# Optimization experiments

Measured on AMD Instinct MI355X. Metric: run time of the kernel, lower is better.

## Reference

```python
import jax, jax.numpy as jnp
import numpy as np

THEA = 0.5
DELTA = 1.5
IGNORE = 255
K = 19  # num classes (len(weights))
LOSS_WEIGHT = 1.0
MIN_PIXELS = 20.0  # class kept only if pixel count > 20
WEIGHTS = jnp.ones((K,), dtype=jnp.float32)
EPS = 1e-12


def setup_inputs() -> dict:
    key = jax.random.key(0)
    k1, k2 = jax.random.split(key)
    n, c, h, w = 4, 32, 512, 1024
    predict = jax.random.normal(k1, (n, c, h, w), dtype=jnp.float32)
    target = jax.random.randint(k2, (n, h, w), 0, K, dtype=jnp.int32)
    return {"predict": predict, "target": target}


def _loss(predict, target):
    n, c, h, w = predict.shape
    # (n,c,h,w) -> (n*h*w, c), matching predict.permute(0,2,3,1)
    feat = jnp.transpose(predict, (0, 2, 3, 1)).reshape(-1, c)
    seg = target.reshape(-1)
    valid_pix = seg != IGNORE
    seg = jnp.where(valid_pix, seg, K).astype(jnp.int32)  # ignored -> extra segment K
    ones = valid_pix.astype(feat.dtype)

    # per-class counts and means (segment reduce replaces the python class loop)
    counts = jax.ops.segment_sum(ones, seg, num_segments=K + 1)[:K]
    sums = jax.ops.segment_sum(feat * ones[:, None], seg, num_segments=K + 1)[:K]
    centers = sums / jnp.maximum(counts, 1.0)[:, None]  # [K, c]
    valid_cls = counts > MIN_PIXELS
    n_cls = jnp.maximum(jnp.sum(valid_cls.astype(feat.dtype)), 1.0)

    # ---- variance term: relu(||mean - x|| - thea)^2, normalized by #positives ----
    ctr_ext = jnp.concatenate([centers, jnp.zeros((1, c), centers.dtype)], axis=0)
    ctr_pix = ctr_ext[seg]  # gather per-pixel center
    res = jnp.sqrt(jnp.sum((ctr_pix - feat) ** 2, axis=1) + EPS)  # [n*h*w]
    r = jax.nn.relu(res - THEA) * ones
    sq = jax.ops.segment_sum(r * r, seg, num_segments=K + 1)[:K]
    pos = jax.ops.segment_sum((r > 0).astype(feat.dtype), seg, num_segments=K + 1)[:K]
    norml = jnp.maximum(jax.lax.stop_gradient(pos), 1.0)  # numpy count in original: no grad
    loss_var = jnp.sum(jnp.where(valid_cls, WEIGHTS * sq / norml, 0.0)) / n_cls

    # ---- pairwise center distance term ----
    diff = centers[:, None, :] - centers[None, :, :]  # [K, K, c]
    dist = jnp.sqrt(jnp.sum(diff * diff, axis=-1) + EPS)
    pair_mask = valid_cls[:, None] & valid_cls[None, :] & ~jnp.eye(K, dtype=bool)
    d = jax.nn.relu(2.0 * DELTA - dist)
    loss_dis = jnp.sum(jnp.where(pair_mask, d * d, 0.0)) / jnp.maximum(n_cls * (n_cls - 1.0), 1.0)

    # ---- regularization term ----
    loss_reg = jnp.sum(jnp.where(valid_cls, jnp.sqrt(jnp.sum(centers * centers, axis=1) + EPS), 0.0)) / n_cls

    return LOSS_WEIGHT * (loss_var + loss_dis + 0.001 * loss_reg)


def reference(predict, target):
    return _loss(predict, target)
```

## Files before the change

kernel.cpp:

```cpp
#include <hip/hip_runtime.h>


#define K_CLS 19
#define C_CH 32
#define HW_SHIFT 19
#define HW_SIZE (1 << HW_SHIFT)
#define EPSF 1e-12f
#define THEA_F 0.5f
#define TWO_DELTA 3.0f
#define MIN_PIX 20.0f
#define HIST_STRIDE 21

#define OFF_PSUM 0
#define OFF_PCNT 40960
#define OFF_RED  42240
#define OFF_VPART 42880
#define WS_FLOATS (OFF_VPART + 1024 * 64)

typedef const unsigned int __attribute__((address_space(1)))* GP;
typedef unsigned int __attribute__((address_space(3)))* LP;

__device__ __forceinline__ void atomAddF(float* p, float v) {
  unsafeAtomicAdd(p, v);
}

__global__ __launch_bounds__(256) void k_accum(
    const float* __restrict__ pred, const int* __restrict__ tgt,
    float* __restrict__ ws)
{
  __shared__ float s_hist[256 * HIST_STRIDE];
  __shared__ float s_w[4][20];
  const int t = threadIdx.x;
  const int w = t >> 6;
  float* hb = &s_hist[t * HIST_STRIDE];
#pragma unroll
  for (int k = 0; k < HIST_STRIDE; ++k) hb[k] = 0.f;

  if (blockIdx.x < 2048) {
    const int plane = blockIdx.x >> 4;
    const int slab  = blockIdx.x & 15;
    const int n_idx = plane >> 5;
    const int ch    = plane & 31;
    const float* pbase = pred + (((size_t)plane) << HW_SHIFT) + ((size_t)slab << 15);
    const int*   tbase = tgt  + (((size_t)n_idx) << HW_SHIFT) + ((size_t)slab << 15);

    float4 vA = *reinterpret_cast<const float4*>(pbase + t * 4);
    int4   cA = *reinterpret_cast<const int4*>(tbase + t * 4);
#pragma unroll 1
    for (int it = 0; it < 32; ++it) {
      float4 vB; int4 cB;
      if (it + 1 < 32) {
        vB = *reinterpret_cast<const float4*>(pbase + (it + 1) * 1024 + t * 4);
        cB = *reinterpret_cast<const int4*>(tbase + (it + 1) * 1024 + t * 4);
      }
      const float x[4] = {vA.x, vA.y, vA.z, vA.w};
      const int   s[4] = {cA.x, cA.y, cA.z, cA.w};
#pragma unroll
      for (int i = 0; i < 4; ++i) {
        const int slot = min((unsigned)s[i], (unsigned)K_CLS);
        hb[slot] += x[i];
      }
      vA = vB; cA = cB;
    }

    float acc[K_CLS];
#pragma unroll
    for (int k = 0; k < K_CLS; ++k) acc[k] = hb[k];
#pragma unroll
    for (int k = 0; k < K_CLS; ++k) {
      float s = acc[k];
#pragma unroll
      for (int m = 1; m < 64; m <<= 1) s += __shfl_xor(s, m, 64);
      acc[k] = s;
    }
#pragma unroll
    for (int k = 0; k < K_CLS; ++k)
      if ((t & 63) == k) s_w[w][k] = acc[k];
    __syncthreads();
    if (t < K_CLS) {
      const int slot = n_idx * 16 + slab;
      ws[OFF_PSUM + ch * (64 * 20) + slot * 20 + t] =
          s_w[0][t] + s_w[1][t] + s_w[2][t] + s_w[3][t];
    }
  } else {
    const int idx = blockIdx.x - 2048;
    const int n_idx = idx >> 4;
    const int slab  = idx & 15;
    const int* tbase = tgt + (((size_t)n_idx) << HW_SHIFT) + ((size_t)slab << 15);

#pragma unroll 1
    for (int it = 0; it < 32; ++it) {
      const int4 c4 = *reinterpret_cast<const int4*>(tbase + it * 1024 + t * 4);
      const int s[4] = {c4.x, c4.y, c4.z, c4.w};
#pragma unroll
      for (int i = 0; i < 4; ++i) {
        const int slot = min((unsigned)s[i], (unsigned)K_CLS);
        hb[slot] += 1.f;
      }
    }

    float acc[K_CLS];
#pragma unroll
    for (int k = 0; k < K_CLS; ++k) acc[k] = hb[k];
#pragma unroll
    for (int k = 0; k < K_CLS; ++k) {
      float s = acc[k];
#pragma unroll
      for (int m = 1; m < 64; m <<= 1) s += __shfl_xor(s, m, 64);
      acc[k] = s;
    }
#pragma unroll
    for (int k = 0; k < K_CLS; ++k)
      if ((t & 63) == k) s_w[w][k] = acc[k];
    __syncthreads();
    if (t < K_CLS) {
      const int slot = n_idx * 16 + slab;
      ws[OFF_PCNT + slot * 20 + t] = s_w[0][t] + s_w[1][t] + s_w[2][t] + s_w[3][t];
    }
  }
}

__global__ __launch_bounds__(256) void k_reduce(float* __restrict__ ws)
{
  const int t = threadIdx.x;
  for (int o = t; o < C_CH * K_CLS; o += 256) {
    const int ch = o / K_CLS, k = o - ch * K_CLS;
    float a = 0.f;
#pragma unroll 4
    for (int s = 0; s < 64; ++s) a += ws[OFF_PSUM + ch * (64 * 20) + s * 20 + k];
    ws[OFF_RED + o] = a;
  }
  if (t < K_CLS) {
    float a = 0.f;
#pragma unroll 4
    for (int s = 0; s < 64; ++s) a += ws[OFF_PCNT + s * 20 + t];
    ws[OFF_RED + C_CH * K_CLS + t] = a;
  }
}

__global__ __launch_bounds__(256) void k_var(
    const float* __restrict__ pred, const int* __restrict__ tgt,
    float* __restrict__ ws)
{
  __shared__ float s_buf[4][2][C_CH][64];
  __shared__ int   s_cls[4][2][256];
  __shared__ float s_ctr[C_CH][K_CLS];
  __shared__ float s_sq[K_CLS];
  __shared__ float s_pos[K_CLS];

  const int t = threadIdx.x;
  const int w = t >> 6;
  const int lane = t & 63;

  for (int i = t; i < C_CH * K_CLS; i += 256) {
    const int k = i % K_CLS;
    (&s_ctr[0][0])[i] = ws[OFF_RED + i] / fmaxf(ws[OFF_RED + C_CH * K_CLS + k], 1.f);
  }
  if (t < K_CLS) { s_sq[t] = 0.f; s_pos[t] = 0.f; }
  __syncthreads();

  const size_t P0 = (size_t)blockIdx.x * 2048;
  const int n_idx = (int)(P0 >> HW_SHIFT);
  const int hw0 = (int)(P0 & (HW_SIZE - 1));
  const int qch = lane >> 4;
  const int qpx = (lane & 15) * 4;

#define STAGE(h, j)                                                           \
  {                                                                           \
    const int pw = hw0 + w * 512 + (j) * 64;                                  \
    _Pragma("unroll")                                                         \
    for (int q = 0; q < 8; ++q) {                                             \
      const int c = q * 4 + qch;                                              \
      const float* gp = pred + (((size_t)(n_idx * C_CH + c)) << HW_SHIFT)     \
                        + pw + qpx;                                           \
      __builtin_amdgcn_global_load_lds((GP)gp, (LP)&s_buf[w][h][0][0] + q * 256, \
                                       16, 0, 0);                             \
    }                                                                         \
    const int* gt = tgt + (((size_t)n_idx) << HW_SHIFT) + pw + qpx;           \
    __builtin_amdgcn_global_load_lds((GP)gt, (LP)&s_cls[w][h][0], 16, 0, 0);  \
  }

  float res8[8];
  int   cls8[8];

  STAGE(0, 0)
#pragma unroll 1
  for (int j = 0; j < 8; ++j) {
    const int h = j & 1;
    if (j < 7) {
      STAGE(h ^ 1, j + 1)
      asm volatile("s_waitcnt vmcnt(9)" ::: "memory");
    } else {
      asm volatile("s_waitcnt vmcnt(0)" ::: "memory");
    }
    __builtin_amdgcn_sched_barrier(0);

    const int ci = s_cls[w][h][lane];
    const bool vld = (unsigned)ci < K_CLS;
    const int sc = vld ? ci : 0;
    float d2 = 0.f;
#pragma unroll
    for (int c = 0; c < C_CH; ++c) {
      const float x = s_buf[w][h][c][lane];
      const float d = s_ctr[c][sc] - x;
      d2 = fmaf(d, d, d2);
    }
    res8[j] = d2;
    cls8[j] = vld ? ci : -1;
  }

#pragma unroll
  for (int j = 0; j < 8; ++j) {
    if (cls8[j] >= 0) {
      const float r = sqrtf(res8[j] + EPSF) - THEA_F;
      if (r > 0.f) { atomAddF(&s_sq[cls8[j]], r * r); atomAddF(&s_pos[cls8[j]], 1.f); }
    }
  }

  __syncthreads();
  if (t < K_CLS) {
    float* vp = ws + OFF_VPART + (size_t)blockIdx.x * 64;
    vp[t]         = s_sq[t];
    vp[K_CLS + t] = s_pos[t];
  }
#undef STAGE
}

__global__ __launch_bounds__(1024) void k_final(
    float* __restrict__ ws, float* __restrict__ out, int nb)
{
  __shared__ float s_ctr[C_CH * K_CLS];
  __shared__ float s_valid[K_CLS];
  __shared__ float s_sq[K_CLS];
  __shared__ float s_pos[K_CLS];
  __shared__ float s_red[3];
  __shared__ float s_ncls;
  const int t = threadIdx.x;
  if (t < 3) s_red[t] = 0.f;
  if (t < K_CLS) { s_sq[t] = 0.f; s_pos[t] = 0.f; }
  if (t < K_CLS) s_valid[t] = (ws[OFF_RED + C_CH * K_CLS + t] > MIN_PIX) ? 1.f : 0.f;
  for (int i = t; i < C_CH * K_CLS; i += 1024) {
    const int k = i % K_CLS;
    s_ctr[i] = ws[OFF_RED + i] / fmaxf(ws[OFF_RED + C_CH * K_CLS + k], 1.f);
  }
  __syncthreads();

  {
    const int o = t & 63, slice = t >> 6;
    if (o < 2 * K_CLS) {
      float a = 0.f;
      for (int b = slice; b < nb; b += 16)
        a += ws[OFF_VPART + (size_t)b * 64 + o];
      atomAddF(o < K_CLS ? &s_sq[o] : &s_pos[o - K_CLS], a);
    }
  }
  __syncthreads();

  if (t == 0) {
    float n = 0.f;
    for (int k = 0; k < K_CLS; ++k) n += s_valid[k];
    s_ncls = fmaxf(n, 1.f);
  }
  if (t < K_CLS && s_valid[t] > 0.f) {
    atomAddF(&s_red[0], s_sq[t] / fmaxf(s_pos[t], 1.f));
    float nn = 0.f;
#pragma unroll
    for (int ch = 0; ch < C_CH; ++ch) {
      const float cv = s_ctr[ch * K_CLS + t];
      nn = fmaf(cv, cv, nn);
    }
    atomAddF(&s_red[2], sqrtf(nn + EPSF));
  }
  if (t < K_CLS * K_CLS) {
    const int a = t / K_CLS, b = t - (t / K_CLS) * K_CLS;
    if (a != b && s_valid[a] > 0.f && s_valid[b] > 0.f) {
      float dd = 0.f;
#pragma unroll
      for (int ch = 0; ch < C_CH; ++ch) {
        const float df = s_ctr[ch * K_CLS + a] - s_ctr[ch * K_CLS + b];
        dd = fmaf(df, df, dd);
      }
      const float dist = sqrtf(dd + EPSF);
      const float d = fmaxf(TWO_DELTA - dist, 0.f);
      if (d > 0.f) atomAddF(&s_red[1], d * d);
    }
  }
  __syncthreads();
  if (t == 0) {
    const float n = s_ncls;
    out[0] = s_red[0] / n
           + s_red[1] / fmaxf(n * (n - 1.f), 1.f)
           + 0.001f * s_red[2] / n;
  }
}

extern "C" void kernel_launch(void* const* d_in, const int* in_sizes, int n_in,
                              void* d_out, int out_size, void* d_ws, size_t ws_size,
                              hipStream_t stream) {
  const float* pred = (const float*)d_in[0];
  const int*   tgt  = (const int*)d_in[1];
  float* ws  = (float*)d_ws;
  float* out = (float*)d_out;
  const int P = in_sizes[1];
  const int nBlocksVar = P / 2048;

  k_accum <<<2048 + 64, 256, 0, stream>>>(pred, tgt, ws);
  k_reduce<<<1, 256, 0, stream>>>(ws);
  k_var   <<<nBlocksVar, 256, 0, stream>>>(pred, tgt, ws);
  k_final <<<1, 1024, 0, stream>>>(ws, out, nBlocksVar);
}
```

Before: 498.2 us.

## Replace LDS-staged variance kernel with direct register loads and per-thread histograms

The variance kernel drops the double-buffered global_load_lds staging. Each thread now loads 4 pixels across all 32 channels straight into registers as float4, and blocks are halved to 1024 pixels each. Shared-memory float atomics are replaced by per-thread column histograms that are reduced with wave shuffles. The accumulation kernel's histogram layout is also changed to a class-major [wave][class][lane] form to avoid bank conflicts. The new variance path relies on many independent loads per thread and doubles the block count, at the cost of higher register pressure and more partial results for the final kernel.

Result: slower. 583.5 us (+17.1%).

```diff
diff --git a/kernel.cpp b/kernel.cpp
--- a/kernel.cpp
+++ b/kernel.cpp
@@ -9,16 +9,12 @@
 #define THEA_F 0.5f
 #define TWO_DELTA 3.0f
 #define MIN_PIX 20.0f
-#define HIST_STRIDE 21
 
 #define OFF_PSUM 0
 #define OFF_PCNT 40960
 #define OFF_RED  42240
 #define OFF_VPART 42880
-#define WS_FLOATS (OFF_VPART + 1024 * 64)
-
-typedef const unsigned int __attribute__((address_space(1)))* GP;
-typedef unsigned int __attribute__((address_space(3)))* LP;
+#define WS_FLOATS (OFF_VPART + 2048 * 64)
 
 __device__ __forceinline__ void atomAddF(float* p, float v) {
   unsafeAtomicAdd(p, v);
@@ -28,13 +24,14 @@
     const float* __restrict__ pred, const int* __restrict__ tgt,
     float* __restrict__ ws)
 {
-  __shared__ float s_hist[256 * HIST_STRIDE];
+  __shared__ float s_hist[4][20][64];
   __shared__ float s_w[4][20];
   const int t = threadIdx.x;
   const int w = t >> 6;
-  float* hb = &s_hist[t * HIST_STRIDE];
-#pragma unroll
-  for (int k = 0; k < HIST_STRIDE; ++k) hb[k] = 0.f;
+  const int lane = t & 63;
+  float* col = &s_hist[w][0][lane];
+#pragma unroll
+  for (int k = 0; k < 20; ++k) col[k << 6] = 0.f;
 
   if (blockIdx.x < 2048) {
     const int plane = blockIdx.x >> 4;
@@ -58,14 +55,14 @@
 #pragma unroll
       for (int i = 0; i < 4; ++i) {
         const int slot = min((unsigned)s[i], (unsigned)K_CLS);
-        hb[slot] += x[i];
+        col[slot << 6] += x[i];
       }
       vA = vB; cA = cB;
     }
 
     float acc[K_CLS];
 #pragma unroll
-    for (int k = 0; k < K_CLS; ++k) acc[k] = hb[k];
+    for (int k = 0; k < K_CLS; ++k) acc[k] = col[k << 6];
 #pragma unroll
     for (int k = 0; k < K_CLS; ++k) {
       float s = acc[k];
@@ -75,7 +72,7 @@
     }
 #pragma unroll
     for (int k = 0; k < K_CLS; ++k)
-      if ((t & 63) == k) s_w[w][k] = acc[k];
+      if (lane == k) s_w[w][k] = acc[k];
     __syncthreads();
     if (t < K_CLS) {
       const int slot = n_idx * 16 + slab;
@@ -95,13 +92,13 @@
 #pragma unroll
       for (int i = 0; i < 4; ++i) {
         const int slot = min((unsigned)s[i], (unsigned)K_CLS);
-        hb[slot] += 1.f;
+        col[slot << 6] += 1.f;
       }
     }
 
     float acc[K_CLS];
 #pragma unroll
-    for (int k = 0; k < K_CLS; ++k) acc[k] = hb[k];
+    for (int k = 0; k < K_CLS; ++k) acc[k] = col[k << 6];
 #pragma unroll
     for (int k = 0; k < K_CLS; ++k) {
       float s = acc[k];
@@ -111,7 +108,7 @@
     }
 #pragma unroll
     for (int k = 0; k < K_CLS; ++k)
-      if ((t & 63) == k) s_w[w][k] = acc[k];
+      if (lane == k) s_w[w][k] = acc[k];
     __syncthreads();
     if (t < K_CLS) {
       const int slot = n_idx * 16 + slab;
@@ -142,88 +139,95 @@
     const float* __restrict__ pred, const int* __restrict__ tgt,
     float* __restrict__ ws)
 {
-  __shared__ float s_buf[4][2][C_CH][64];
-  __shared__ int   s_cls[4][2][256];
-  __shared__ float s_ctr[C_CH][K_CLS];
-  __shared__ float s_sq[K_CLS];
-  __shared__ float s_pos[K_CLS];
+  __shared__ float s_ctrT[K_CLS][36];
+  __shared__ float s_sq[20][256];
+  __shared__ float s_pos[20][256];
+  __shared__ float s_w[4][20];
+  __shared__ float s_w2[4][20];
 
   const int t = threadIdx.x;
   const int w = t >> 6;
   const int lane = t & 63;
 
   for (int i = t; i < C_CH * K_CLS; i += 256) {
-    const int k = i % K_CLS;
-    (&s_ctr[0][0])[i] = ws[OFF_RED + i] / fmaxf(ws[OFF_RED + C_CH * K_CLS + k], 1.f);
-  }
-  if (t < K_CLS) { s_sq[t] = 0.f; s_pos[t] = 0.f; }
-  __syncthreads();
-
-  const size_t P0 = (size_t)blockIdx.x * 2048;
+    const int c = i / K_CLS, s = i - c * K_CLS;
+    s_ctrT[s][c] = ws[OFF_RED + i] / fmaxf(ws[OFF_RED + C_CH * K_CLS + s], 1.f);
+  }
+  for (int i = t; i < 20 * 256; i += 256) {
+    (&s_sq[0][0])[i] = 0.f;
+    (&s_pos[0][0])[i] = 0.f;
+  }
+  __syncthreads();
+
+  const size_t P0 = (size_t)blockIdx.x * 1024;
   const int n_idx = (int)(P0 >> HW_SHIFT);
-  const int hw0 = (int)(P0 & (HW_SIZE - 1));
-  const int qch = lane >> 4;
-  const int qpx = (lane & 15) * 4;
-
-#define STAGE(h, j)                                                           \
-  {                                                                           \
-    const int pw = hw0 + w * 512 + (j) * 64;                                  \
-    _Pragma("unroll")                                                         \
-    for (int q = 0; q < 8; ++q) {                                             \
-      const int c = q * 4 + qch;                                              \
-      const float* gp = pred + (((size_t)(n_idx * C_CH + c)) << HW_SHIFT)     \
-                        + pw + qpx;                                           \
-      __builtin_amdgcn_global_load_lds((GP)gp, (LP)&s_buf[w][h][0][0] + q * 256, \
-                                       16, 0, 0);                             \
-    }                                                                         \
-    const int* gt = tgt + (((size_t)n_idx) << HW_SHIFT) + pw + qpx;           \
-    __builtin_amdgcn_global_load_lds((GP)gt, (LP)&s_cls[w][h][0], 16, 0, 0);  \
-  }
-
-  float res8[8];
-  int   cls8[8];
-
-  STAGE(0, 0)
-#pragma unroll 1
-  for (int j = 0; j < 8; ++j) {
-    const int h = j & 1;
-    if (j < 7) {
-      STAGE(h ^ 1, j + 1)
-      asm volatile("s_waitcnt vmcnt(9)" ::: "memory");
-    } else {
-      asm volatile("s_waitcnt vmcnt(0)" ::: "memory");
-    }
-    __builtin_amdgcn_sched_barrier(0);
-
-    const int ci = s_cls[w][h][lane];
-    const bool vld = (unsigned)ci < K_CLS;
-    const int sc = vld ? ci : 0;
-    float d2 = 0.f;
-#pragma unroll
-    for (int c = 0; c < C_CH; ++c) {
-      const float x = s_buf[w][h][c][lane];
-      const float d = s_ctr[c][sc] - x;
-      d2 = fmaf(d, d, d2);
-    }
-    res8[j] = d2;
-    cls8[j] = vld ? ci : -1;
-  }
-
-#pragma unroll
-  for (int j = 0; j < 8; ++j) {
-    if (cls8[j] >= 0) {
-      const float r = sqrtf(res8[j] + EPSF) - THEA_F;
-      if (r > 0.f) { atomAddF(&s_sq[cls8[j]], r * r); atomAddF(&s_pos[cls8[j]], 1.f); }
-    }
-  }
-
+  const int hw = (int)(P0 & (HW_SIZE - 1)) + w * 256 + lane * 4;
+  const float* pb = pred + (((size_t)(n_idx * C_CH)) << HW_SHIFT) + hw;
+
+  const int4 c4 = *reinterpret_cast<const int4*>(tgt + (((size_t)n_idx) << HW_SHIFT) + hw);
+  int  sc[4] = {c4.x, c4.y, c4.z, c4.w};
+  bool vl[4];
+#pragma unroll
+  for (int j = 0; j < 4; ++j) { vl[j] = (unsigned)sc[j] < K_CLS; if (!vl[j]) sc[j] = 0; }
+
+  float4 xv[C_CH];
+#pragma unroll
+  for (int c = 0; c < C_CH; ++c)
+    xv[c] = *reinterpret_cast<const float4*>(pb + ((size_t)c << HW_SHIFT));
+
+  float d2[4] = {0.f, 0.f, 0.f, 0.f};
+#pragma unroll
+  for (int j = 0; j < 4; ++j) {
+    const int s = sc[j];
+#pragma unroll
+    for (int cb = 0; cb < 8; ++cb) {
+      const float4 g = *reinterpret_cast<const float4*>(&s_ctrT[s][cb * 4]);
+      const float x0 = ((const float*)&xv[cb * 4 + 0])[j];
+      const float x1 = ((const float*)&xv[cb * 4 + 1])[j];
+      const float x2 = ((const float*)&xv[cb * 4 + 2])[j];
+      const float x3 = ((const float*)&xv[cb * 4 + 3])[j];
+      const float e0 = g.x - x0, e1 = g.y - x1, e2 = g.z - x2, e3 = g.w - x3;
+      d2[j] = fmaf(e0, e0, d2[j]);
+      d2[j] = fmaf(e1, e1, d2[j]);
+      d2[j] = fmaf(e2, e2, d2[j]);
+      d2[j] = fmaf(e3, e3, d2[j]);
+    }
+  }
+
+#pragma unroll
+  for (int j = 0; j < 4; ++j) {
+    if (vl[j]) {
+      const float r = sqrtf(d2[j] + EPSF) - THEA_F;
+      if (r > 0.f) {
+        s_sq[sc[j]][t]  += r * r;
+        s_pos[sc[j]][t] += 1.f;
+      }
+    }
+  }
+
+  __syncthreads();
+  float asq[K_CLS], apos[K_CLS];
+#pragma unroll
+  for (int k = 0; k < K_CLS; ++k) { asq[k] = s_sq[k][t]; apos[k] = s_pos[k][t]; }
+#pragma unroll
+  for (int k = 0; k < K_CLS; ++k) {
+    float a = asq[k], b = apos[k];
+#pragma unroll
+    for (int m = 1; m < 64; m <<= 1) {
+      a += __shfl_xor(a, m, 64);
+      b += __shfl_xor(b, m, 64);
+    }
+    asq[k] = a; apos[k] = b;
+  }
+#pragma unroll
+  for (int k = 0; k < K_CLS; ++k)
+    if (lane == k) { s_w[w][k] = asq[k]; s_w2[w][k] = apos[k]; }
   __syncthreads();
   if (t < K_CLS) {
     float* vp = ws + OFF_VPART + (size_t)blockIdx.x * 64;
-    vp[t]         = s_sq[t];
-    vp[K_CLS + t] = s_pos[t];
-  }
-#undef STAGE
+    vp[t]         = s_w[0][t] + s_w[1][t] + s_w[2][t] + s_w[3][t];
+    vp[K_CLS + t] = s_w2[0][t] + s_w2[1][t] + s_w2[2][t] + s_w2[3][t];
+  }
 }
 
 __global__ __launch_bounds__(1024) void k_final(
@@ -302,7 +306,7 @@
   float* ws  = (float*)d_ws;
   float* out = (float*)d_out;
   const int P = in_sizes[1];
-  const int nBlocksVar = P / 2048;
+  const int nBlocksVar = P / 1024;
 
   k_accum <<<2048 + 64, 256, 0, stream>>>(pred, tgt, ws);
   k_reduce<<<1, 256, 0, stream>>>(ws);
```

## Bank-friendly split LDS histograms and parallelize small reductions across many blocks

Applied to the files above, without the earlier changes.

The per-thread strided LDS histogram is replaced with per-wave column-major histograms, split into two alternating copies so consecutive updates do not depend on each other. Ignored pixels now add zero to a clamped slot, which removes the extra bin. The single-block k_reduce becomes one 64-lane block per output using wave shuffles. The per-block variance partials are reduced by a new multi-block k_vred kernel instead of inside k_final. Together these aim to cut LDS bank conflicts and the serial tails, at the cost of one extra kernel launch. The new k_vred hardcodes 1024 var blocks.

Result: faster. 449.6 us (-9.8%).

```diff
diff --git a/kernel.cpp b/kernel.cpp
--- a/kernel.cpp
+++ b/kernel.cpp
@@ -9,12 +9,12 @@
 #define THEA_F 0.5f
 #define TWO_DELTA 3.0f
 #define MIN_PIX 20.0f
-#define HIST_STRIDE 21
 
 #define OFF_PSUM 0
 #define OFF_PCNT 40960
 #define OFF_RED  42240
-#define OFF_VPART 42880
+#define OFF_VRED 42880
+#define OFF_VPART 42944
 #define WS_FLOATS (OFF_VPART + 1024 * 64)
 
 typedef const unsigned int __attribute__((address_space(1)))* GP;
@@ -28,13 +28,16 @@
     const float* __restrict__ pred, const int* __restrict__ tgt,
     float* __restrict__ ws)
 {
-  __shared__ float s_hist[256 * HIST_STRIDE];
+  __shared__ float sA[4][K_CLS][64];
+  __shared__ float sB[4][K_CLS][64];
   __shared__ float s_w[4][20];
   const int t = threadIdx.x;
   const int w = t >> 6;
-  float* hb = &s_hist[t * HIST_STRIDE];
-#pragma unroll
-  for (int k = 0; k < HIST_STRIDE; ++k) hb[k] = 0.f;
+  const int lane = t & 63;
+  float* colA = &sA[w][0][lane];
+  float* colB = &sB[w][0][lane];
+#pragma unroll
+  for (int k = 0; k < K_CLS; ++k) { colA[k << 6] = 0.f; colB[k << 6] = 0.f; }
 
   if (blockIdx.x < 2048) {
     const int plane = blockIdx.x >> 4;
@@ -55,17 +58,22 @@
       }
       const float x[4] = {vA.x, vA.y, vA.z, vA.w};
       const int   s[4] = {cA.x, cA.y, cA.z, cA.w};
-#pragma unroll
-      for (int i = 0; i < 4; ++i) {
-        const int slot = min((unsigned)s[i], (unsigned)K_CLS);
-        hb[slot] += x[i];
-      }
+      const int   k0 = min((unsigned)s[0], 18u), k1 = min((unsigned)s[1], 18u);
+      const int   k2 = min((unsigned)s[2], 18u), k3 = min((unsigned)s[3], 18u);
+      const float v0 = ((unsigned)s[0] < K_CLS) ? x[0] : 0.f;
+      const float v1 = ((unsigned)s[1] < K_CLS) ? x[1] : 0.f;
+      const float v2 = ((unsigned)s[2] < K_CLS) ? x[2] : 0.f;
+      const float v3 = ((unsigned)s[3] < K_CLS) ? x[3] : 0.f;
+      colA[k0 << 6] += v0;
+      colB[k1 << 6] += v1;
+      colA[k2 << 6] += v2;
+      colB[k3 << 6] += v3;
       vA = vB; cA = cB;
     }
 
     float acc[K_CLS];
 #pragma unroll
-    for (int k = 0; k < K_CLS; ++k) acc[k] = hb[k];
+    for (int k = 0; k < K_CLS; ++k) acc[k] = colA[k << 6] + colB[k << 6];
 #pragma unroll
     for (int k = 0; k < K_CLS; ++k) {
       float s = acc[k];
@@ -75,7 +83,7 @@
     }
 #pragma unroll
     for (int k = 0; k < K_CLS; ++k)
-      if ((t & 63) == k) s_w[w][k] = acc[k];
+      if (lane == k) s_w[w][k] = acc[k];
     __syncthreads();
     if (t < K_CLS) {
       const int slot = n_idx * 16 + slab;
@@ -92,16 +100,17 @@
     for (int it = 0; it < 32; ++it) {
       const int4 c4 = *reinterpret_cast<const int4*>(tbase + it * 1024 + t * 4);
       const int s[4] = {c4.x, c4.y, c4.z, c4.w};
-#pragma unroll
-      for (int i = 0; i < 4; ++i) {
-        const int slot = min((unsigned)s[i], (unsigned)K_CLS);
-        hb[slot] += 1.f;
-      }
+      const int k0 = min((unsigned)s[0], 18u), k1 = min((unsigned)s[1], 18u);
+      const int k2 = min((unsigned)s[2], 18u), k3 = min((unsigned)s[3], 18u);
+      colA[k0 << 6] += ((unsigned)s[0] < K_CLS) ? 1.f : 0.f;
+      colB[k1 << 6] += ((unsigned)s[1] < K_CLS) ? 1.f : 0.f;
+      colA[k2 << 6] += ((unsigned)s[2] < K_CLS) ? 1.f : 0.f;
+      colB[k3 << 6] += ((unsigned)s[3] < K_CLS) ? 1.f : 0.f;
     }
 
     float acc[K_CLS];
 #pragma unroll
-    for (int k = 0; k < K_CLS; ++k) acc[k] = hb[k];
+    for (int k = 0; k < K_CLS; ++k) acc[k] = colA[k << 6] + colB[k << 6];
 #pragma unroll
     for (int k = 0; k < K_CLS; ++k) {
       float s = acc[k];
@@ -111,7 +120,7 @@
     }
 #pragma unroll
     for (int k = 0; k < K_CLS; ++k)
-      if ((t & 63) == k) s_w[w][k] = acc[k];
+      if (lane == k) s_w[w][k] = acc[k];
     __syncthreads();
     if (t < K_CLS) {
       const int slot = n_idx * 16 + slab;
@@ -120,22 +129,20 @@
   }
 }
 
-__global__ __launch_bounds__(256) void k_reduce(float* __restrict__ ws)
-{
-  const int t = threadIdx.x;
-  for (int o = t; o < C_CH * K_CLS; o += 256) {
+__global__ __launch_bounds__(64) void k_reduce(float* __restrict__ ws)
+{
+  const int o = blockIdx.x;
+  const int lane = threadIdx.x;
+  float a;
+  if (o < C_CH * K_CLS) {
     const int ch = o / K_CLS, k = o - ch * K_CLS;
-    float a = 0.f;
-#pragma unroll 4
-    for (int s = 0; s < 64; ++s) a += ws[OFF_PSUM + ch * (64 * 20) + s * 20 + k];
-    ws[OFF_RED + o] = a;
-  }
-  if (t < K_CLS) {
-    float a = 0.f;
-#pragma unroll 4
-    for (int s = 0; s < 64; ++s) a += ws[OFF_PCNT + s * 20 + t];
-    ws[OFF_RED + C_CH * K_CLS + t] = a;
-  }
+    a = ws[OFF_PSUM + ch * (64 * 20) + lane * 20 + k];
+  } else {
+    a = ws[OFF_PCNT + lane * 20 + (o - C_CH * K_CLS)];
+  }
+#pragma unroll
+  for (int m = 1; m < 64; m <<= 1) a += __shfl_xor(a, m, 64);
+  if (lane == 0) ws[OFF_RED + o] = a;
 }
 
 __global__ __launch_bounds__(256) void k_var(
@@ -226,18 +233,31 @@
 #undef STAGE
 }
 
+__global__ __launch_bounds__(256) void k_vred(float* __restrict__ ws)
+{
+  const int o = blockIdx.x;
+  const int t = threadIdx.x;
+  float a = 0.f;
+#pragma unroll
+  for (int r = 0; r < 4; ++r)
+    a += ws[OFF_VPART + (size_t)(t + r * 256) * 64 + o];
+#pragma unroll
+  for (int m = 1; m < 64; m <<= 1) a += __shfl_xor(a, m, 64);
+  __shared__ float s[4];
+  if ((t & 63) == 0) s[t >> 6] = a;
+  __syncthreads();
+  if (t == 0) ws[OFF_VRED + o] = s[0] + s[1] + s[2] + s[3];
+}
+
 __global__ __launch_bounds__(1024) void k_final(
-    float* __restrict__ ws, float* __restrict__ out, int nb)
+    float* __restrict__ ws, float* __restrict__ out)
 {
   __shared__ float s_ctr[C_CH * K_CLS];
   __shared__ float s_valid[K_CLS];
-  __shared__ float s_sq[K_CLS];
-  __shared__ float s_pos[K_CLS];
   __shared__ float s_red[3];
   __shared__ float s_ncls;
   const int t = threadIdx.x;
   if (t < 3) s_red[t] = 0.f;
-  if (t < K_CLS) { s_sq[t] = 0.f; s_pos[t] = 0.f; }
   if (t < K_CLS) s_valid[t] = (ws[OFF_RED + C_CH * K_CLS + t] > MIN_PIX) ? 1.f : 0.f;
   for (int i = t; i < C_CH * K_CLS; i += 1024) {
     const int k = i % K_CLS;
@@ -245,24 +265,15 @@
   }
   __syncthreads();
 
-  {
-    const int o = t & 63, slice = t >> 6;
-    if (o < 2 * K_CLS) {
-      float a = 0.f;
-      for (int b = slice; b < nb; b += 16)
-        a += ws[OFF_VPART + (size_t)b * 64 + o];
-      atomAddF(o < K_CLS ? &s_sq[o] : &s_pos[o - K_CLS], a);
-    }
-  }
-  __syncthreads();
-
   if (t == 0) {
     float n = 0.f;
     for (int k = 0; k < K_CLS; ++k) n += s_valid[k];
     s_ncls = fmaxf(n, 1.f);
   }
   if (t < K_CLS && s_valid[t] > 0.f) {
-    atomAddF(&s_red[0], s_sq[t] / fmaxf(s_pos[t], 1.f));
+    const float sq  = ws[OFF_VRED + t];
+    const float pos = ws[OFF_VRED + K_CLS + t];
+    atomAddF(&s_red[0], sq / fmaxf(pos, 1.f));
     float nn = 0.f;
 #pragma unroll
     for (int ch = 0; ch < C_CH; ++ch) {
@@ -305,7 +316,8 @@
   const int nBlocksVar = P / 2048;
 
   k_accum <<<2048 + 64, 256, 0, stream>>>(pred, tgt, ws);
-  k_reduce<<<1, 256, 0, stream>>>(ws);
+  k_reduce<<<C_CH * K_CLS + K_CLS, 64, 0, stream>>>(ws);
   k_var   <<<nBlocksVar, 256, 0, stream>>>(pred, tgt, ws);
-  k_final <<<1, 1024, 0, stream>>>(ws, out, nBlocksVar);
-}
+  k_vred  <<<2 * K_CLS, 256, 0, stream>>>(ws);
+  k_final <<<1, 1024, 0, stream>>>(ws, out);
+}
```
